# Kernel optimization log

Hardware: AMD Instinct MI355X
Metric: run time of the kernel (lower is better)

Reference implementation:

```python
import jax, jax.numpy as jnp
import numpy as np

B, R, C, NH, G = 32, 64, 96, 3, 8   # batch, patches_resolution, dim, heads, group(window) size
HD = C // NH                         # head dim = 32
SCALE = HD ** -0.5
HID = 4 * C                          # mlp hidden = mlp_ratio * dim


def setup_inputs() -> dict:
    key = jax.random.key(0)
    ks = jax.random.split(key, 16)
    n = jax.random.normal
    s = 0.02
    return {
        "x": n(ks[0], (B, R * R, C), jnp.float32),
        "w_qkv": n(ks[1], (C, 3 * C), jnp.float32) * s,
        "b_qkv": jnp.zeros((3 * C,), jnp.float32),
        "w_lepe": n(ks[2], (C, 1, 3, 3), jnp.float32) * s,  # depthwise conv, OIHW with groups=C
        "b_lepe": jnp.zeros((C,), jnp.float32),
        "w_proj": n(ks[3], (C, C), jnp.float32) * s,
        "b_proj": jnp.zeros((C,), jnp.float32),
        "g1": jnp.ones((C,), jnp.float32),
        "bt1": jnp.zeros((C,), jnp.float32),
        "g2": jnp.ones((C,), jnp.float32),
        "bt2": jnp.zeros((C,), jnp.float32),
        "w_fc1": n(ks[4], (C, HID), jnp.float32) * s,
        "b_fc1": jnp.zeros((HID,), jnp.float32),
        "w_fc2": n(ks[5], (HID, C), jnp.float32) * s,
        "b_fc2": jnp.zeros((C,), jnp.float32),
    }


def _ln(x, g, b):
    m = x.mean(-1, keepdims=True)
    v = ((x - m) ** 2).mean(-1, keepdims=True)
    return (x - m) * jax.lax.rsqrt(v + 1e-5) * g + b


def reference(x, w_qkv, b_qkv, w_lepe, b_lepe, w_proj, b_proj,
              g1, bt1, g2, bt2, w_fc1, b_fc1, w_fc2, b_fc2):
    Bn, L, _ = x.shape
    H = W = R
    shortcut = x
    # norm1 + SDA window partition: (B,H,W,C) -> (B*nW, G*G, C)
    h = _ln(x, g1, bt1).reshape(Bn, H // G, G, W // G, G, C)
    h = h.transpose(0, 1, 3, 2, 4, 5).reshape(-1, G * G, C)
    B_ = h.shape[0]
    qkv = (h @ w_qkv + b_qkv).reshape(B_, G * G, 3, NH, HD).transpose(2, 0, 3, 1, 4)
    q, k, v = qkv[0], qkv[1], qkv[2]            # (B_, NH, G*G, HD)
    # LePE: depthwise 3x3 conv on V viewed as (B_, C, G, G)
    vimg = v.transpose(0, 1, 3, 2).reshape(B_, C, G, G)
    lepe = jax.lax.conv_general_dilated(
        vimg, w_lepe, window_strides=(1, 1), padding='SAME',
        feature_group_count=C, dimension_numbers=('NCHW', 'OIHW', 'NCHW'))
    lepe = lepe + b_lepe[None, :, None, None]
    lepe = lepe.reshape(B_, NH, HD, G * G).transpose(0, 1, 3, 2)  # (B_, NH, G*G, HD)
    # attention (no mask registered in this block)
    attn = jax.nn.softmax((q * SCALE) @ k.transpose(0, 1, 3, 2), axis=-1)
    o = (attn @ v + lepe).transpose(0, 2, 1, 3).reshape(B_, G * G, C)
    o = o @ w_proj + b_proj
    # window reverse
    o = o.reshape(Bn, H // G, W // G, G, G, C).transpose(0, 1, 3, 2, 4, 5).reshape(Bn, L, C)
    x1 = shortcut + o
    # MLP block (exact GELU, as torch nn.GELU default)
    m = _ln(x1, g2, bt2)
    m = jax.nn.gelu(m @ w_fc1 + b_fc1, approximate=False) @ w_fc2 + b_fc2
    return (x1 + m, attn)
```

## Files before the change

kernel.cpp:

```cpp
#include <hip/hip_runtime.h>
#include <hip/hip_bf16.h>

typedef short short8 __attribute__((ext_vector_type(8)));
typedef float f32x4 __attribute__((ext_vector_type(4)));

constexpr int BDIM = 32, RDIM = 64, CDIM = 96, NH_ = 3, HD_ = 32;
constexpr int LTOK = RDIM * RDIM;
constexpr int GG = 64;
constexpr int HID = 384;
constexpr int NWIN = 2048;
constexpr float SCALE = 0.17677669529663687f;
constexpr long OUT1OFF = (long)BDIM * LTOK * CDIM;

constexpr int O_WQKVT = 0;
constexpr int O_WPROJT = 27648;
constexpr int O_WFC1T = 36864;
constexpr int O_WFC2T = 73728;
constexpr int W_TOT = 110592;

__device__ __forceinline__ unsigned short f2b(float f) {
  return __builtin_bit_cast(unsigned short, __float2bfloat16(f));
}
__device__ __forceinline__ float b2f(unsigned short u) {
  return __bfloat162float(__builtin_bit_cast(__hip_bfloat16, u));
}

__device__ __forceinline__ float gelu_f(float x) {
  float u = x * 0.70710678118654752f;
  float ax = __builtin_fabsf(u);
  float t = __builtin_amdgcn_rcpf(1.f + 0.3275911f * ax);
  float poly = t * (0.254829592f +
               t * (-0.284496736f +
               t * (1.421413741f +
               t * (-1.453152027f +
               t * 1.061405429f))));
  float erf_abs = 1.f - poly * __expf(-ax * ax);
  float erf_u = (u < 0.f) ? -erf_abs : erf_abs;
  return 0.5f * x * (1.f + erf_u);
}

__global__ void prep_weights(const float* __restrict__ wqkv,
                             const float* __restrict__ wproj,
                             const float* __restrict__ wfc1,
                             const float* __restrict__ wfc2,
                             unsigned short* __restrict__ ws) {
  int i = blockIdx.x * 256 + threadIdx.x;
  if (i >= W_TOT) return;
  float v;
  if (i < O_WPROJT) {
    int n = i / 96, k = i - n * 96;
    v = wqkv[k * 288 + n];
  } else if (i < O_WFC1T) {
    int j = i - O_WPROJT, n = j / 96, k = j - n * 96;
    v = wproj[k * 96 + n];
  } else if (i < O_WFC2T) {
    int j = i - O_WFC1T, n = j / 96, k = j - n * 96;
    v = wfc1[k * 384 + n];
  } else {
    int j = i - O_WFC2T, n = j / 384, k = j - n * 384;
    v = wfc2[k * 96 + n];
  }
  ws[i] = f2b(v);
}

__global__ __launch_bounds__(256, 2)
void attn_mfma(const float* __restrict__ x, const float* __restrict__ bqkv,
               const float* __restrict__ wlepe, const float* __restrict__ blepe,
               const float* __restrict__ bproj, const float* __restrict__ g1,
               const float* __restrict__ bt1,
               const unsigned short* __restrict__ ws, float* __restrict__ out) {
  constexpr int SA = 104;
  constexpr int SQ = 200;
  constexpr int SV = 72;
  constexpr int SP = 72;
  __shared__ __attribute__((aligned(16))) unsigned short hA[64 * SA];
  __shared__ __attribute__((aligned(16))) unsigned short qkS[64 * SQ];
  __shared__ __attribute__((aligned(16))) unsigned short vS[96 * SV];
  __shared__ __attribute__((aligned(16))) unsigned short pS[64 * SP];

  const int tid = threadIdx.x, lane = tid & 63;
  const int wv = __builtin_amdgcn_readfirstlane(tid >> 6);
  const int w = blockIdx.x, b = w >> 6, wi = w & 63, wr = wi >> 3, wc = wi & 7;
  const long xbase = (long)b * (LTOK * CDIM);
  const int l15 = lane & 15, lk = (lane >> 4) * 8, lr = (lane >> 4) * 4;
  const int p = lane >> 4;
  const int tok = wv * 16 + l15;

  {
    const long rowbase =
        xbase + (long)((wr * 8 + (tok >> 3)) * RDIM + wc * 8 + (tok & 7)) * CDIM;
    const float* rb = x + rowbase + p * 24;
    float xv[24], s1 = 0.f, s2 = 0.f;
#pragma unroll
    for (int i = 0; i < 6; ++i) {
      f32x4 v4 = *(const f32x4*)(rb + i * 4);
#pragma unroll
      for (int j = 0; j < 4; ++j) {
        float v = v4[j];
        xv[i * 4 + j] = v; s1 += v; s2 += v * v;
      }
    }
    s1 += __shfl_xor(s1, 16, 64); s1 += __shfl_xor(s1, 32, 64);
    s2 += __shfl_xor(s2, 16, 64); s2 += __shfl_xor(s2, 32, 64);
    float m = s1 * (1.f / 96.f);
    float vv = s2 * (1.f / 96.f) - m * m;
    float rs = rsqrtf(vv + 1e-5f);
    unsigned short tmp[24];
#pragma unroll
    for (int i = 0; i < 6; ++i) {
      f32x4 gv = *(const f32x4*)(g1 + p * 24 + i * 4);
      f32x4 bv = *(const f32x4*)(bt1 + p * 24 + i * 4);
#pragma unroll
      for (int j = 0; j < 4; ++j)
        tmp[i * 4 + j] = f2b((xv[i * 4 + j] - m) * rs * gv[j] + bv[j]);
    }
#pragma unroll
    for (int i = 0; i < 3; ++i)
      *(short8*)&hA[tok * SA + p * 24 + i * 8] = *(const short8*)&tmp[i * 8];
  }

  {
    f32x4 acc[18];
#pragma unroll
    for (int t = 0; t < 18; ++t) acc[t] = (f32x4){0.f, 0.f, 0.f, 0.f};
    const int arow = wv * 16 + l15;
    __builtin_amdgcn_s_setprio(1);
#pragma unroll
    for (int kk = 0; kk < 3; ++kk) {
      short8 a = *(const short8*)&hA[arow * SA + kk * 32 + lk];
#pragma unroll
      for (int nt = 0; nt < 18; ++nt) {
        short8 bw = *(const short8*)&ws[O_WQKVT + (nt * 16 + l15) * 96 + kk * 32 + lk];
        acc[nt] = __builtin_amdgcn_mfma_f32_16x16x32_bf16(a, bw, acc[nt], 0, 0, 0);
      }
    }
    __builtin_amdgcn_s_setprio(0);
#pragma unroll
    for (int nt = 0; nt < 18; ++nt) {
      int n0 = nt * 16 + l15;
      float bias = bqkv[n0];
#pragma unroll
      for (int r = 0; r < 4; ++r) {
        int tk = wv * 16 + lr + r;
        float v = acc[nt][r] + bias;
        if (n0 < 96) qkS[tk * SQ + n0] = f2b(v * SCALE);
        else if (n0 < 192) qkS[tk * SQ + n0] = f2b(v);
        else vS[(n0 - 192) * SV + tk] = f2b(v);
      }
    }
  }
  __syncthreads();

  if (tid < 192) {
    const int c = tid >> 1;
    const int half = tid & 1;
    const int r0 = half * 4;
    float rowb[6][8];
#pragma unroll
    for (int rr = 0; rr < 6; ++rr) {
      int vr = r0 - 1 + rr;
      if (vr >= 0 && vr < 8) {
        short8 v8 = *(const short8*)&vS[c * SV + vr * 8];
#pragma unroll
        for (int j = 0; j < 8; ++j) rowb[rr][j] = b2f((unsigned short)v8[j]);
      } else {
#pragma unroll
        for (int j = 0; j < 8; ++j) rowb[rr][j] = 0.f;
      }
    }
    float lw9[9];
#pragma unroll
    for (int q = 0; q < 9; ++q) lw9[q] = wlepe[c * 9 + q];
    const float lb = blepe[c];
#pragma unroll
    for (int r = 0; r < 4; ++r) {
#pragma unroll
      for (int cc = 0; cc < 8; ++cc) {
        float a = lb;
#pragma unroll
        for (int kh = 0; kh < 3; ++kh) {
          const float* rbp = rowb[r + kh];
          if (cc > 0) a += lw9[kh * 3 + 0] * rbp[cc - 1];
          a += lw9[kh * 3 + 1] * rbp[cc];
          if (cc < 7) a += lw9[kh * 3 + 2] * rbp[cc + 1];
        }
        hA[((r0 + r) * 8 + cc) * SA + c] = f2b(a);
      }
    }
  }
  __syncthreads();

  for (int h = 0; h < NH_; ++h) {
    f32x4 sacc[4];
#pragma unroll
    for (int t = 0; t < 4; ++t) sacc[t] = (f32x4){0.f, 0.f, 0.f, 0.f};
    short8 aq = *(const short8*)&qkS[(wv * 16 + l15) * SQ + h * 32 + lk];
#pragma unroll
    for (int nt = 0; nt < 4; ++nt) {
      short8 bk = *(const short8*)&qkS[(nt * 16 + l15) * SQ + 96 + h * 32 + lk];
      sacc[nt] = __builtin_amdgcn_mfma_f32_16x16x32_bf16(aq, bk, sacc[nt], 0, 0, 0);
    }
    float pr[4][4];
#pragma unroll
    for (int r = 0; r < 4; ++r) {
      float mx = -1e30f;
#pragma unroll
      for (int nt = 0; nt < 4; ++nt) mx = fmaxf(mx, sacc[nt][r]);
#pragma unroll
      for (int s = 1; s < 16; s <<= 1) mx = fmaxf(mx, __shfl_xor(mx, s, 64));
      float sum = 0.f;
#pragma unroll
      for (int nt = 0; nt < 4; ++nt) {
        float e = __expf(sacc[nt][r] - mx);
        pr[nt][r] = e; sum += e;
      }
#pragma unroll
      for (int s = 1; s < 16; s <<= 1) sum += __shfl_xor(sum, s, 64);
      float inv = 1.f / sum;
#pragma unroll
      for (int nt = 0; nt < 4; ++nt) pr[nt][r] *= inv;
    }
    const long o1base = OUT1OFF + ((long)(w * NH_ + h) * GG) * GG;
#pragma unroll
    for (int nt = 0; nt < 4; ++nt) {
      int col = nt * 16 + l15;
#pragma unroll
      for (int r = 0; r < 4; ++r) {
        int row = wv * 16 + lr + r;
        out[o1base + (long)row * GG + col] = pr[nt][r];
        pS[row * SP + col] = f2b(pr[nt][r]);
      }
    }
    f32x4 oa[2];
    oa[0] = (f32x4){0.f, 0.f, 0.f, 0.f};
    oa[1] = (f32x4){0.f, 0.f, 0.f, 0.f};
#pragma unroll
    for (int kk = 0; kk < 2; ++kk) {
      short8 ap = *(const short8*)&pS[(wv * 16 + l15) * SP + kk * 32 + lk];
#pragma unroll
      for (int nt = 0; nt < 2; ++nt) {
        short8 bv = *(const short8*)&vS[(h * 32 + nt * 16 + l15) * SV + kk * 32 + lk];
        oa[nt] = __builtin_amdgcn_mfma_f32_16x16x32_bf16(ap, bv, oa[nt], 0, 0, 0);
      }
    }
#pragma unroll
    for (int nt = 0; nt < 2; ++nt) {
      int c = h * 32 + nt * 16 + l15;
#pragma unroll
      for (int r = 0; r < 4; ++r) {
        int tk = wv * 16 + lr + r;
        hA[tk * SA + c] = f2b(oa[nt][r] + b2f(hA[tk * SA + c]));
      }
    }
  }

  {
    f32x4 pacc[6];
#pragma unroll
    for (int t = 0; t < 6; ++t) pacc[t] = (f32x4){0.f, 0.f, 0.f, 0.f};
    __builtin_amdgcn_s_setprio(1);
#pragma unroll
    for (int kk = 0; kk < 3; ++kk) {
      short8 ao = *(const short8*)&hA[(wv * 16 + l15) * SA + kk * 32 + lk];
#pragma unroll
      for (int nt = 0; nt < 6; ++nt) {
        short8 bw = *(const short8*)&ws[O_WPROJT + (nt * 16 + l15) * 96 + kk * 32 + lk];
        pacc[nt] = __builtin_amdgcn_mfma_f32_16x16x32_bf16(ao, bw, pacc[nt], 0, 0, 0);
      }
    }
    __builtin_amdgcn_s_setprio(0);
#pragma unroll
    for (int nt = 0; nt < 6; ++nt) {
      int ch = nt * 16 + l15;
      float bias = bproj[ch];
#pragma unroll
      for (int r = 0; r < 4; ++r) {
        int tk = wv * 16 + lr + r;
        long g = xbase + (long)((wr * 8 + (tk >> 3)) * RDIM + wc * 8 + (tk & 7)) * CDIM + ch;
        out[g] = x[g] + pacc[nt][r] + bias;
      }
    }
  }
}

__global__ __launch_bounds__(256)
void mlp_mfma(const float* __restrict__ bfc1, const float* __restrict__ bfc2,
              const float* __restrict__ g2, const float* __restrict__ bt2,
              const unsigned short* __restrict__ ws, float* __restrict__ out) {
  constexpr int SB = 104;
  constexpr int SHQ = 104;
  __shared__ __attribute__((aligned(16))) unsigned short hB[64 * SB];
  __shared__ __attribute__((aligned(16))) unsigned short Hq[64 * SHQ];

  const int tid = threadIdx.x, lane = tid & 63;
  const int wv = __builtin_amdgcn_readfirstlane(tid >> 6);
  const long t0 = (long)blockIdx.x * GG;
  const int l15 = lane & 15, lk = (lane >> 4) * 8, lr = (lane >> 4) * 4;
  const int p = lane >> 4;
  const int tok = wv * 16 + l15;

  {
    const float* rb = out + (t0 + tok) * CDIM + p * 24;
    float xv[24], s1 = 0.f, s2 = 0.f;
#pragma unroll
    for (int i = 0; i < 6; ++i) {
      f32x4 v4 = *(const f32x4*)(rb + i * 4);
#pragma unroll
      for (int j = 0; j < 4; ++j) {
        float v = v4[j];
        xv[i * 4 + j] = v; s1 += v; s2 += v * v;
      }
    }
    s1 += __shfl_xor(s1, 16, 64); s1 += __shfl_xor(s1, 32, 64);
    s2 += __shfl_xor(s2, 16, 64); s2 += __shfl_xor(s2, 32, 64);
    float m = s1 * (1.f / 96.f);
    float vv = s2 * (1.f / 96.f) - m * m;
    float rs = rsqrtf(vv + 1e-5f);
    unsigned short tmp[24];
#pragma unroll
    for (int i = 0; i < 24; ++i) {
      int c = p * 24 + i;
      tmp[i] = f2b((xv[i] - m) * rs * g2[c] + bt2[c]);
    }
#pragma unroll
    for (int i = 0; i < 3; ++i)
      *(short8*)&hB[tok * SB + p * 24 + i * 8] = *(const short8*)&tmp[i * 8];
  }

  f32x4 acc2[6];
#pragma unroll
  for (int t = 0; t < 6; ++t) acc2[t] = (f32x4){0.f, 0.f, 0.f, 0.f};

#pragma unroll 1
  for (int q = 0; q < 4; ++q) {
    f32x4 acc1[6];
#pragma unroll
    for (int t = 0; t < 6; ++t) acc1[t] = (f32x4){0.f, 0.f, 0.f, 0.f};
#pragma unroll
    for (int kk = 0; kk < 3; ++kk) {
      short8 a = *(const short8*)&hB[(wv * 16 + l15) * SB + kk * 32 + lk];
#pragma unroll
      for (int nt = 0; nt < 6; ++nt) {
        int n = q * 96 + nt * 16 + l15;
        short8 bw = *(const short8*)&ws[O_WFC1T + n * 96 + kk * 32 + lk];
        acc1[nt] = __builtin_amdgcn_mfma_f32_16x16x32_bf16(a, bw, acc1[nt], 0, 0, 0);
      }
    }
#pragma unroll
    for (int nt = 0; nt < 6; ++nt) {
      int n = q * 96 + nt * 16 + l15;
      float bias = bfc1[n];
#pragma unroll
      for (int r = 0; r < 4; ++r) {
        int tk = wv * 16 + lr + r;
        Hq[tk * SHQ + nt * 16 + l15] = f2b(gelu_f(acc1[nt][r] + bias));
      }
    }
#pragma unroll
    for (int kk = 0; kk < 3; ++kk) {
      short8 a = *(const short8*)&Hq[(wv * 16 + l15) * SHQ + kk * 32 + lk];
#pragma unroll
      for (int nt = 0; nt < 6; ++nt) {
        short8 bw = *(const short8*)&ws[O_WFC2T + (nt * 16 + l15) * 384 + q * 96 + kk * 32 + lk];
        acc2[nt] = __builtin_amdgcn_mfma_f32_16x16x32_bf16(a, bw, acc2[nt], 0, 0, 0);
      }
    }
  }

#pragma unroll
  for (int nt = 0; nt < 6; ++nt) {
    int ch = nt * 16 + l15;
    float bias = bfc2[ch];
#pragma unroll
    for (int r = 0; r < 4; ++r) {
      int tk = wv * 16 + lr + r;
      long g = (t0 + tk) * CDIM + ch;
      out[g] = out[g] + acc2[nt][r] + bias;
    }
  }
}

struct PF {
  const float *x, *w_qkv, *b_qkv, *w_lepe, *b_lepe, *w_proj, *b_proj;
  const float *g1, *bt1, *g2, *bt2, *w_fc1, *b_fc1, *w_fc2, *b_fc2;
  float* out;
};

__global__ __launch_bounds__(256, 2)
void attn_scalar(PF p) {
  constexpr int SA = 66;
  __shared__ __hip_bfloat16 bufA[CDIM * SA];
  __shared__ __hip_bfloat16 qkvT[288 * GG];
  __shared__ __hip_bfloat16 sPad[GG * SA];
  __shared__ float meanS[GG], rstdS[GG];

  const int w = blockIdx.x;
  const int b = w >> 6, wi = w & 63, wr = wi >> 3, wc = wi & 7;
  const int tid = threadIdx.x, lane = tid & 63;
  const int wv = __builtin_amdgcn_readfirstlane(tid >> 6);
  const long xbase = (long)b * (LTOK * CDIM);

  for (int k = 0; k < 24; ++k) {
    int e = tid + k * 256, wrow = e / 768, o = e - wrow * 768;
    int tir = o / 96, ch = o - tir * 96;
    long g = xbase + ((wr * 8 + wrow) * RDIM + wc * 8 + tir) * CDIM + ch;
    bufA[ch * SA + wrow * 8 + tir] = __float2bfloat16(p.x[g]);
  }
  __syncthreads();
  if (wv == 0) {
    float m = 0.f;
    for (int c = 0; c < CDIM; ++c) m += __bfloat162float(bufA[c * SA + lane]);
    m *= (1.f / CDIM);
    float var = 0.f;
    for (int c = 0; c < CDIM; ++c) {
      float d = __bfloat162float(bufA[c * SA + lane]) - m;
      var += d * d;
    }
    meanS[lane] = m;
    rstdS[lane] = rsqrtf(var * (1.f / CDIM) + 1e-5f);
  }
  __syncthreads();
  {
    float m = meanS[lane], rs = rstdS[lane];
    for (int cc = 0; cc < 24; ++cc) {
      int c = wv * 24 + cc;
      float v = __bfloat162float(bufA[c * SA + lane]);
      bufA[c * SA + lane] = __float2bfloat16((v - m) * rs * p.g1[c] + p.bt1[c]);
    }
  }
  __syncthreads();
  for (int tile = 0; tile < 2; ++tile) {
    int j0 = wv * 72 + tile * 36;
    float acc[36];
#pragma unroll
    for (int jj = 0; jj < 36; ++jj) acc[jj] = p.b_qkv[j0 + jj];
#pragma unroll 1
    for (int c = 0; c < CDIM; ++c) {
      float hv = __bfloat162float(bufA[c * SA + lane]);
#pragma unroll
      for (int jj = 0; jj < 36; ++jj) acc[jj] += hv * p.w_qkv[c * 288 + j0 + jj];
    }
#pragma unroll
    for (int jj = 0; jj < 36; ++jj)
      qkvT[(j0 + jj) * GG + lane] = __float2bfloat16(acc[jj]);
  }
  __syncthreads();
  for (int hh = 0; hh < NH_; ++hh) {
    float kreg[HD_];
#pragma unroll
    for (int d = 0; d < HD_; ++d)
      kreg[d] = __bfloat162float(qkvT[(CDIM + hh * HD_ + d) * GG + lane]);
#pragma unroll 1
    for (int r = 0; r < 16; ++r) {
      int i = wv * 16 + r;
      float acc = 0.f;
#pragma unroll
      for (int d = 0; d < HD_; ++d)
        acc += __bfloat162float(qkvT[(hh * HD_ + d) * GG + i]) * kreg[d];
      sPad[lane * SA + i] = __float2bfloat16(acc * SCALE);
    }
#pragma unroll 1
    for (int r = 0; r < 16; ++r) {
      int i = wv * 16 + r;
      float v = __bfloat162float(sPad[lane * SA + i]);
      float mx = v;
#pragma unroll
      for (int s = 32; s > 0; s >>= 1) mx = fmaxf(mx, __shfl_xor(mx, s, 64));
      float e = __expf(v - mx);
      float sum = e;
#pragma unroll
      for (int s = 32; s > 0; s >>= 1) sum += __shfl_xor(sum, s, 64);
      float rr = e / sum;
      sPad[lane * SA + i] = __float2bfloat16(rr);
      p.out[OUT1OFF + ((long)(w * NH_ + hh) * GG + i) * GG + lane] = rr;
    }
    __syncthreads();
    {
      int d0 = wv * 8;
      float acc[8];
#pragma unroll
      for (int dd = 0; dd < 8; ++dd) acc[dd] = 0.f;
#pragma unroll 1
      for (int j = 0; j < GG; ++j) {
        float sv = __bfloat162float(sPad[j * SA + lane]);
#pragma unroll
        for (int dd = 0; dd < 8; ++dd)
          acc[dd] += sv * __bfloat162float(qkvT[(2 * CDIM + hh * HD_ + d0 + dd) * GG + j]);
      }
      int tr = lane >> 3, tc = lane & 7;
#pragma unroll
      for (int dd = 0; dd < 8; ++dd) {
        int c = hh * HD_ + d0 + dd;
        float a = p.b_lepe[c];
#pragma unroll
        for (int kh = 0; kh < 3; ++kh)
#pragma unroll
          for (int kw = 0; kw < 3; ++kw) {
            int rr2 = tr + kh - 1, cc2 = tc + kw - 1;
            if (rr2 >= 0 && rr2 < 8 && cc2 >= 0 && cc2 < 8)
              a += p.w_lepe[c * 9 + kh * 3 + kw] *
                   __bfloat162float(qkvT[(2 * CDIM + hh * HD_ + d0 + dd) * GG + rr2 * 8 + cc2]);
          }
        acc[dd] += a;
      }
#pragma unroll
      for (int dd = 0; dd < 8; ++dd)
        bufA[(hh * HD_ + d0 + dd) * SA + lane] = __float2bfloat16(acc[dd]);
    }
    __syncthreads();
  }
  __hip_bfloat16* projT = qkvT;
  {
    int j0 = wv * 24;
    float acc[24];
#pragma unroll
    for (int jj = 0; jj < 24; ++jj) acc[jj] = p.b_proj[j0 + jj];
#pragma unroll 1
    for (int c = 0; c < CDIM; ++c) {
      float ov = __bfloat162float(bufA[c * SA + lane]);
#pragma unroll
      for (int jj = 0; jj < 24; ++jj) acc[jj] += ov * p.w_proj[c * CDIM + j0 + jj];
    }
#pragma unroll
    for (int jj = 0; jj < 24; ++jj)
      projT[(j0 + jj) * SA + lane] = __float2bfloat16(acc[jj]);
  }
  __syncthreads();
  for (int k = 0; k < 24; ++k) {
    int e = tid + k * 256, wrow = e / 768, o = e - wrow * 768;
    int tir = o / 96, ch = o - tir * 96;
    long g = xbase + ((wr * 8 + wrow) * RDIM + wc * 8 + tir) * CDIM + ch;
    p.out[g] = p.x[g] + __bfloat162float(projT[ch * SA + wrow * 8 + tir]);
  }
}

__global__ __launch_bounds__(256, 2)
void mlp_scalar(PF p) {
  constexpr int SB = 66;
  __shared__ __hip_bfloat16 bufB[CDIM * SB];
  __shared__ __hip_bfloat16 hidT[HID * GG];
  __shared__ float meanS[GG], rstdS[GG];

  const int tid = threadIdx.x, lane = tid & 63;
  const int wv = __builtin_amdgcn_readfirstlane(tid >> 6);
  const long t0 = (long)blockIdx.x * GG;

  for (int k = 0; k < 24; ++k) {
    int e = tid + k * 256, tok = e / 96, ch = e - tok * 96;
    bufB[ch * SB + tok] = __float2bfloat16(p.out[(t0 + tok) * CDIM + ch]);
  }
  __syncthreads();
  if (wv == 0) {
    float m = 0.f;
    for (int c = 0; c < CDIM; ++c) m += __bfloat162float(bufB[c * SB + lane]);
    m *= (1.f / CDIM);
    float var = 0.f;
    for (int c = 0; c < CDIM; ++c) {
      float d = __bfloat162float(bufB[c * SB + lane]) - m;
      var += d * d;
    }
    meanS[lane] = m;
    rstdS[lane] = rsqrtf(var * (1.f / CDIM) + 1e-5f);
  }
  __syncthreads();
  {
    float m = meanS[lane], rs = rstdS[lane];
    for (int cc = 0; cc < 24; ++cc) {
      int c = wv * 24 + cc;
      float v = __bfloat162float(bufB[c * SB + lane]);
      bufB[c * SB + lane] = __float2bfloat16((v - m) * rs * p.g2[c] + p.bt2[c]);
    }
  }
  __syncthreads();
  for (int tile = 0; tile < 4; ++tile) {
    int j0 = wv * 96 + tile * 24;
    float acc[24];
#pragma unroll
    for (int jj = 0; jj < 24; ++jj) acc[jj] = p.b_fc1[j0 + jj];
#pragma unroll 1
    for (int c = 0; c < CDIM; ++c) {
      float hv = __bfloat162float(bufB[c * SB + lane]);
#pragma unroll
      for (int jj = 0; jj < 24; ++jj) acc[jj] += hv * p.w_fc1[c * HID + j0 + jj];
    }
#pragma unroll
    for (int jj = 0; jj < 24; ++jj) {
      float xg = acc[jj];
      hidT[(j0 + jj) * GG + lane] =
          __float2bfloat16(0.5f * xg * (1.f + erff(xg * 0.70710678118f)));
    }
  }
  __syncthreads();
  {
    int j0 = wv * 24;
    float acc[24];
#pragma unroll
    for (int jj = 0; jj < 24; ++jj) acc[jj] = p.b_fc2[j0 + jj];
#pragma unroll 1
    for (int h = 0; h < HID; ++h) {
      float hv = __bfloat162float(hidT[h * GG + lane]);
#pragma unroll
      for (int jj = 0; jj < 24; ++jj) acc[jj] += hv * p.w_fc2[h * CDIM + j0 + jj];
    }
#pragma unroll
    for (int jj = 0; jj < 24; ++jj)
      bufB[(j0 + jj) * SB + lane] = __float2bfloat16(acc[jj]);
  }
  __syncthreads();
  for (int k = 0; k < 24; ++k) {
    int e = tid + k * 256, tok = e / 96, ch = e - tok * 96;
    long g = (t0 + tok) * CDIM + ch;
    p.out[g] = p.out[g] + __bfloat162float(bufB[ch * SB + tok]);
  }
}

extern "C" void kernel_launch(void* const* d_in, const int* in_sizes, int n_in,
                              void* d_out, int out_size, void* d_ws, size_t ws_size,
                              hipStream_t stream) {
  const float* x = (const float*)d_in[0];
  const float* w_qkv = (const float*)d_in[1];
  const float* b_qkv = (const float*)d_in[2];
  const float* w_lepe = (const float*)d_in[3];
  const float* b_lepe = (const float*)d_in[4];
  const float* w_proj = (const float*)d_in[5];
  const float* b_proj = (const float*)d_in[6];
  const float* g1 = (const float*)d_in[7];
  const float* bt1 = (const float*)d_in[8];
  const float* g2 = (const float*)d_in[9];
  const float* bt2 = (const float*)d_in[10];
  const float* w_fc1 = (const float*)d_in[11];
  const float* b_fc1 = (const float*)d_in[12];
  const float* w_fc2 = (const float*)d_in[13];
  const float* b_fc2 = (const float*)d_in[14];
  float* out = (float*)d_out;
  const int mlp_blocks = (BDIM * LTOK) / GG;

  if (ws_size >= (size_t)W_TOT * sizeof(unsigned short)) {
    unsigned short* ws = (unsigned short*)d_ws;
    prep_weights<<<(W_TOT + 255) / 256, 256, 0, stream>>>(w_qkv, w_proj, w_fc1, w_fc2, ws);
    attn_mfma<<<NWIN, 256, 0, stream>>>(x, b_qkv, w_lepe, b_lepe, b_proj, g1, bt1, ws, out);
    mlp_mfma<<<mlp_blocks, 256, 0, stream>>>(b_fc1, b_fc2, g2, bt2, ws, out);
  } else {
    PF p{x, w_qkv, b_qkv, w_lepe, b_lepe, w_proj, b_proj,
         g1, bt1, g2, bt2, w_fc1, b_fc1, w_fc2, b_fc2, out};
    attn_scalar<<<NWIN, 256, 0, stream>>>(p);
    mlp_scalar<<<mlp_blocks, 256, 0, stream>>>(p);
  }
}
```

Measured before the change: 389.8 us.

## Fuse MLP into the windowed attention kernel, keeping x1 in registers

Merges the attention and MLP kernels into one per-window kernel. The proj output plus residual stays in MFMA accumulator registers, LayerNorm2 is computed with cross-lane shuffles, and the fc1/GELU/fc2 chain runs in the same block. This avoids writing x1 to global memory and reading it back, and saves one kernel launch. In exchange the fused kernel needs more registers and LDS (an extra Hq buffer) under launch_bounds(256,2), which could cut occupancy or cause spills.

```diff
diff --git a/kernel.cpp b/kernel.cpp
--- a/kernel.cpp
+++ b/kernel.cpp
@@ -64,19 +64,23 @@
 }
 
 __global__ __launch_bounds__(256, 2)
-void attn_mfma(const float* __restrict__ x, const float* __restrict__ bqkv,
-               const float* __restrict__ wlepe, const float* __restrict__ blepe,
-               const float* __restrict__ bproj, const float* __restrict__ g1,
-               const float* __restrict__ bt1,
-               const unsigned short* __restrict__ ws, float* __restrict__ out) {
+void attn_mlp_mfma(const float* __restrict__ x, const float* __restrict__ bqkv,
+                   const float* __restrict__ wlepe, const float* __restrict__ blepe,
+                   const float* __restrict__ bproj, const float* __restrict__ g1,
+                   const float* __restrict__ bt1, const float* __restrict__ g2,
+                   const float* __restrict__ bt2, const float* __restrict__ bfc1,
+                   const float* __restrict__ bfc2,
+                   const unsigned short* __restrict__ ws, float* __restrict__ out) {
   constexpr int SA = 104;
   constexpr int SQ = 200;
   constexpr int SV = 72;
   constexpr int SP = 72;
+  constexpr int SHQ = 104;
   __shared__ __attribute__((aligned(16))) unsigned short hA[64 * SA];
   __shared__ __attribute__((aligned(16))) unsigned short qkS[64 * SQ];
   __shared__ __attribute__((aligned(16))) unsigned short vS[96 * SV];
   __shared__ __attribute__((aligned(16))) unsigned short pS[64 * SP];
+  __shared__ __attribute__((aligned(16))) unsigned short Hq[64 * SHQ];
 
   const int tid = threadIdx.x, lane = tid & 63;
   const int wv = __builtin_amdgcn_readfirstlane(tid >> 6);
@@ -254,10 +258,10 @@
     }
   }
 
+  f32x4 pacc[6];
+#pragma unroll
+  for (int t = 0; t < 6; ++t) pacc[t] = (f32x4){0.f, 0.f, 0.f, 0.f};
   {
-    f32x4 pacc[6];
-#pragma unroll
-    for (int t = 0; t < 6; ++t) pacc[t] = (f32x4){0.f, 0.f, 0.f, 0.f};
     __builtin_amdgcn_s_setprio(1);
 #pragma unroll
     for (int kk = 0; kk < 3; ++kk) {
@@ -269,62 +273,47 @@
       }
     }
     __builtin_amdgcn_s_setprio(0);
-#pragma unroll
-    for (int nt = 0; nt < 6; ++nt) {
-      int ch = nt * 16 + l15;
-      float bias = bproj[ch];
-#pragma unroll
-      for (int r = 0; r < 4; ++r) {
-        int tk = wv * 16 + lr + r;
-        long g = xbase + (long)((wr * 8 + (tk >> 3)) * RDIM + wc * 8 + (tk & 7)) * CDIM + ch;
-        out[g] = x[g] + pacc[nt][r] + bias;
-      }
-    }
-  }
-}
-
-__global__ __launch_bounds__(256)
-void mlp_mfma(const float* __restrict__ bfc1, const float* __restrict__ bfc2,
-              const float* __restrict__ g2, const float* __restrict__ bt2,
-              const unsigned short* __restrict__ ws, float* __restrict__ out) {
-  constexpr int SB = 104;
-  constexpr int SHQ = 104;
-  __shared__ __attribute__((aligned(16))) unsigned short hB[64 * SB];
-  __shared__ __attribute__((aligned(16))) unsigned short Hq[64 * SHQ];
-
-  const int tid = threadIdx.x, lane = tid & 63;
-  const int wv = __builtin_amdgcn_readfirstlane(tid >> 6);
-  const long t0 = (long)blockIdx.x * GG;
-  const int l15 = lane & 15, lk = (lane >> 4) * 8, lr = (lane >> 4) * 4;
-  const int p = lane >> 4;
-  const int tok = wv * 16 + l15;
-
-  {
-    const float* rb = out + (t0 + tok) * CDIM + p * 24;
-    float xv[24], s1 = 0.f, s2 = 0.f;
-#pragma unroll
-    for (int i = 0; i < 6; ++i) {
-      f32x4 v4 = *(const f32x4*)(rb + i * 4);
-#pragma unroll
-      for (int j = 0; j < 4; ++j) {
-        float v = v4[j];
-        xv[i * 4 + j] = v; s1 += v; s2 += v * v;
-      }
-    }
-    s1 += __shfl_xor(s1, 16, 64); s1 += __shfl_xor(s1, 32, 64);
-    s2 += __shfl_xor(s2, 16, 64); s2 += __shfl_xor(s2, 32, 64);
+  }
+
+  long grow[4];
+#pragma unroll
+  for (int r = 0; r < 4; ++r) {
+    int tk = wv * 16 + lr + r;
+    grow[r] = xbase + (long)((wr * 8 + (tk >> 3)) * RDIM + wc * 8 + (tk & 7)) * CDIM;
+  }
+#pragma unroll
+  for (int nt = 0; nt < 6; ++nt) {
+    int ch = nt * 16 + l15;
+    float bias = bproj[ch];
+#pragma unroll
+    for (int r = 0; r < 4; ++r)
+      pacc[nt][r] = x[grow[r] + ch] + pacc[nt][r] + bias;
+  }
+
+  float m4[4], rs4[4];
+#pragma unroll
+  for (int r = 0; r < 4; ++r) {
+    float s1 = 0.f, s2 = 0.f;
+#pragma unroll
+    for (int nt = 0; nt < 6; ++nt) { float v = pacc[nt][r]; s1 += v; s2 += v * v; }
+#pragma unroll
+    for (int s = 1; s < 16; s <<= 1) {
+      s1 += __shfl_xor(s1, s, 64);
+      s2 += __shfl_xor(s2, s, 64);
+    }
     float m = s1 * (1.f / 96.f);
     float vv = s2 * (1.f / 96.f) - m * m;
-    float rs = rsqrtf(vv + 1e-5f);
-    unsigned short tmp[24];
-#pragma unroll
-    for (int i = 0; i < 24; ++i) {
-      int c = p * 24 + i;
-      tmp[i] = f2b((xv[i] - m) * rs * g2[c] + bt2[c]);
-    }
-#pragma unroll
-    for (int i = 0; i < 3; ++i)
-      *(short8*)&hB[tok * SB + p * 24 + i * 8] = *(const short8*)&tmp[i * 8];
+    m4[r] = m; rs4[r] = rsqrtf(vv + 1e-5f);
+  }
+#pragma unroll
+  for (int nt = 0; nt < 6; ++nt) {
+    int ch = nt * 16 + l15;
+    float gg = g2[ch], bb = bt2[ch];
+#pragma unroll
+    for (int r = 0; r < 4; ++r) {
+      int tk = wv * 16 + lr + r;
+      hA[tk * SA + ch] = f2b((pacc[nt][r] - m4[r]) * rs4[r] * gg + bb);
+    }
   }
 
   f32x4 acc2[6];
@@ -338,7 +327,7 @@
     for (int t = 0; t < 6; ++t) acc1[t] = (f32x4){0.f, 0.f, 0.f, 0.f};
 #pragma unroll
     for (int kk = 0; kk < 3; ++kk) {
-      short8 a = *(const short8*)&hB[(wv * 16 + l15) * SB + kk * 32 + lk];
+      short8 a = *(const short8*)&hA[(wv * 16 + l15) * SA + kk * 32 + lk];
 #pragma unroll
       for (int nt = 0; nt < 6; ++nt) {
         int n = q * 96 + nt * 16 + l15;
@@ -372,11 +361,8 @@
     int ch = nt * 16 + l15;
     float bias = bfc2[ch];
 #pragma unroll
-    for (int r = 0; r < 4; ++r) {
-      int tk = wv * 16 + lr + r;
-      long g = (t0 + tk) * CDIM + ch;
-      out[g] = out[g] + acc2[nt][r] + bias;
-    }
+    for (int r = 0; r < 4; ++r)
+      out[grow[r] + ch] = pacc[nt][r] + acc2[nt][r] + bias;
   }
 }
 
@@ -638,8 +624,8 @@
   if (ws_size >= (size_t)W_TOT * sizeof(unsigned short)) {
     unsigned short* ws = (unsigned short*)d_ws;
     prep_weights<<<(W_TOT + 255) / 256, 256, 0, stream>>>(w_qkv, w_proj, w_fc1, w_fc2, ws);
-    attn_mfma<<<NWIN, 256, 0, stream>>>(x, b_qkv, w_lepe, b_lepe, b_proj, g1, bt1, ws, out);
-    mlp_mfma<<<mlp_blocks, 256, 0, stream>>>(b_fc1, b_fc2, g2, bt2, ws, out);
+    attn_mlp_mfma<<<NWIN, 256, 0, stream>>>(x, b_qkv, w_lepe, b_lepe, b_proj,
+                                            g1, bt1, g2, bt2, b_fc1, b_fc2, ws, out);
   } else {
     PF p{x, w_qkv, b_qkv, w_lepe, b_lepe, w_proj, b_proj,
          g1, bt1, g2, bt2, w_fc1, b_fc1, w_fc2, b_fc2, out};
```

Measured after the change: 348.8 us. 10.5% less time.
